# Kernel optimization log

Measured on AMD Instinct MI355X. Metric: run time of the kernel, lower is better.

The kernel has to match this reference:

```python
import jax, jax.numpy as jnp
import numpy as np

C = 128

def setup_inputs() -> dict:
    key = jax.random.key(0)
    ks = jax.random.split(key, 7)
    s = 1.0 / np.sqrt(C)
    return {
        "x": jax.random.normal(ks[0], (8, C, 64, 64), dtype=jnp.float32),
        "Wq": jax.random.uniform(ks[1], (C, C), jnp.float32, -s, s),
        "bq": jax.random.uniform(ks[2], (C,), jnp.float32, -s, s),
        "Wk": jax.random.uniform(ks[3], (C, C), jnp.float32, -s, s),
        "bk": jax.random.uniform(ks[4], (C,), jnp.float32, -s, s),
        "Wv": jax.random.uniform(ks[5], (C, C), jnp.float32, -s, s),
        "bv": jax.random.uniform(ks[6], (C,), jnp.float32, -s, s),
    }

def reference(x, Wq, bq, Wk, bk, Wv, bv):
    bs, c, h, w = x.shape
    xf = x.reshape(bs, c, h * w)                      # [B, C, N]
    # 1x1 convs == per-pixel linear maps over channels
    q = jnp.einsum("dc,bcn->bdn", Wq, xf) + bq[None, :, None]
    k = jnp.einsum("dc,bcn->bdn", Wk, xf) + bk[None, :, None]
    v = jnp.einsum("dc,bcn->bdn", Wv, xf) + bv[None, :, None]
    # energy[b,i,j] = <q[:,i], k[:,j]>  (no 1/sqrt(d) scaling, per original)
    energy = jnp.einsum("bci,bcj->bij", q, k)         # [B, N, N]
    attn = jax.nn.softmax(energy, axis=-1)
    # out[b,c,i] = sum_j v[b,c,j] * attn[b,i,j]
    out = jnp.einsum("bcj,bij->bci", v, attn)
    return out.reshape(bs, c, h, w)
```

## Files before the change

kernel.cpp:

```cpp
#include <hip/hip_runtime.h>
#include <stdint.h>
#include <math.h>

typedef float  f32x2  __attribute__((ext_vector_type(2)));
typedef float  f32x4  __attribute__((ext_vector_type(4)));
typedef float  f32x16 __attribute__((ext_vector_type(16)));
typedef short  bf16x8 __attribute__((ext_vector_type(8)));
typedef unsigned int u32;
typedef unsigned int u32x4 __attribute__((ext_vector_type(4)));
typedef unsigned short ushort_t;

#define MFMA32(a, b, c) __builtin_amdgcn_mfma_f32_32x32x16_bf16((a), (b), (c), 0, 0, 0)

constexpr int B_ = 8, C_ = 128, N_ = 4096;
constexpr float LOG2E = 1.44269504088896340736f;

__device__ __forceinline__ u32 pack2bf(float a, float b) {
  u32 ua = __builtin_bit_cast(u32, a);
  u32 ub = __builtin_bit_cast(u32, b);
  ua += 0x7fffu + ((ua >> 16) & 1u);
  ub += 0x7fffu + ((ub >> 16) & 1u);
  return (ua >> 16) | (ub & 0xffff0000u);
}
__device__ __forceinline__ u32 pkfast(float a, float b) {
  u32 ua = __builtin_bit_cast(u32, a) + 0x8000u;
  u32 ub = __builtin_bit_cast(u32, b) + 0x8000u;
  return __builtin_amdgcn_perm(ub, ua, 0x07060302u);
}
__device__ __forceinline__ bf16x8 pack8(const float* v, float s) {
  u32x4 d = { pack2bf(v[0]*s, v[1]*s), pack2bf(v[2]*s, v[3]*s),
              pack2bf(v[4]*s, v[5]*s), pack2bf(v[6]*s, v[7]*s) };
  return __builtin_bit_cast(bf16x8, d);
}

__device__ __forceinline__ void gload_lds16(const ushort_t* g, ushort_t* l) {
  __builtin_amdgcn_global_load_lds(
      (const __attribute__((address_space(1))) void*)g,
      (__attribute__((address_space(3))) void*)l, 16, 0, 0);
}

__device__ __forceinline__ bf16x8 mk_pa(const f32x16& sv, int rb, float& lacc) {
  float e0 = __builtin_amdgcn_exp2f(sv[rb+0]);
  float e1 = __builtin_amdgcn_exp2f(sv[rb+1]);
  float e2 = __builtin_amdgcn_exp2f(sv[rb+2]);
  float e3 = __builtin_amdgcn_exp2f(sv[rb+3]);
  float e4 = __builtin_amdgcn_exp2f(sv[rb+4]);
  float e5 = __builtin_amdgcn_exp2f(sv[rb+5]);
  float e6 = __builtin_amdgcn_exp2f(sv[rb+6]);
  float e7 = __builtin_amdgcn_exp2f(sv[rb+7]);
  lacc += ((e0+e1)+(e2+e3)) + ((e4+e5)+(e6+e7));
  u32 a  = pkfast(e0, e1), b2 = pkfast(e2, e3);
  u32 c2 = pkfast(e4, e5), d2 = pkfast(e6, e7);
  asm("v_permlane32_swap_b32 %0, %1" : "+v"(a), "+v"(c2));
  asm("v_permlane32_swap_b32 %0, %1" : "+v"(b2), "+v"(d2));
  u32x4 fr = { a, b2, c2, d2 };
  return __builtin_bit_cast(bf16x8, fr);
}

__global__ __launch_bounds__(256)
void wprep_kernel(const float* __restrict__ Wq, const float* __restrict__ Wk,
                  const float* __restrict__ Wv, ushort_t* __restrict__ Wf)
{
  const int tid  = blockIdx.x * 256 + threadIdx.x;
  const int widx = tid >> 11;
  const int r    = tid & 2047;
  const int dt   = r >> 9;
  const int kc   = (r >> 6) & 7;
  const int ln   = r & 63;
  const float* W = (widx == 0) ? Wq : (widx == 1) ? Wk : Wv;
  const float s  = (widx == 0) ? LOG2E : 1.0f;
  const int d    = dt * 32 + (ln & 31);
  const int c0   = kc * 16 + (ln >> 5) * 8;
  const float* p = W + d * C_ + c0;
  f32x4 lo = *(const f32x4*)p, hi = *(const f32x4*)(p + 4);
  float v[8] = { lo.x, lo.y, lo.z, lo.w, hi.x, hi.y, hi.z, hi.w };
  *(bf16x8*)(Wf + (size_t)tid * 8) = pack8(v, s);
}

__global__ __launch_bounds__(256, 3)
void proj_kernel(const float* __restrict__ x,
                 const float* __restrict__ bq, const float* __restrict__ bk,
                 const float* __restrict__ bv, const ushort_t* __restrict__ Wf,
                 ushort_t* __restrict__ Qf, ushort_t* __restrict__ Kf,
                 ushort_t* __restrict__ Vf)
{
  const int b   = blockIdx.x & 7;
  const int nt  = blockIdx.x >> 3;
  const int n0  = nt << 5;
  const int t   = threadIdx.x;
  const int dt  = t >> 6;
  const int lane = t & 63;
  const int l31 = t & 31;
  const int lq1 = (t >> 5) & 1;

  __shared__ float xs[32 * 130];
  {
    const float* xb = x + (size_t)b * C_ * N_ + n0;
    const int m  = t & 7;
    const int cb = t >> 3;
#pragma unroll
    for (int it = 0; it < 4; ++it) {
      const int c = it * 32 + cb;
      f32x4 v = *(const f32x4*)(xb + (size_t)c * N_ + m * 4);
#pragma unroll
      for (int e = 0; e < 4; ++e)
        xs[(m * 4 + e) * 130 + c] = v[e];
    }
  }
  __syncthreads();

  bf16x8 xf[8];
#pragma unroll
  for (int kc = 0; kc < 8; ++kc) {
    const float* row = &xs[l31 * 130 + kc * 16 + lq1 * 8];
    float v[8];
#pragma unroll
    for (int u = 0; u < 4; ++u) {
      f32x2 p = *(const f32x2*)(row + 2 * u);
      v[2*u] = p.x; v[2*u+1] = p.y;
    }
    xf[kc] = pack8(v, 1.0f);
  }

  const ushort_t* WQf = Wf;
  const ushort_t* WKf = Wf + 16384;
  const ushort_t* WVf = Wf + 32768;
  const f32x16 Z = {0,0,0,0,0,0,0,0,0,0,0,0,0,0,0,0};

  f32x16 sq = Z, sk = Z, sv = Z;
#pragma unroll
  for (int kc = 0; kc < 8; ++kc) {
    const size_t wo = (size_t)(dt * 8 + kc) * 512 + lane * 8;
    bf16x8 wq = *(const bf16x8*)(WQf + wo);
    bf16x8 wk = *(const bf16x8*)(WKf + wo);
    bf16x8 wvv = *(const bf16x8*)(WVf + wo);
    sq = MFMA32(wq, xf[kc], sq);
    sk = MFMA32(wk, xf[kc], sk);
    sv = MFMA32(xf[kc], wvv, sv);
  }

#pragma unroll
  for (int q = 0; q < 4; ++q) {
    const int dbase = dt * 32 + q * 8 + lq1 * 4;
    f32x4 b4q = *(const f32x4*)(bq + dbase);
    f32x4 b4k = *(const f32x4*)(bk + dbase);
    uint2 qs, ks;
    qs.x = pack2bf(sq[4*q+0] + b4q.x * LOG2E, sq[4*q+1] + b4q.y * LOG2E);
    qs.y = pack2bf(sq[4*q+2] + b4q.z * LOG2E, sq[4*q+3] + b4q.w * LOG2E);
    ks.x = pack2bf(sk[4*q+0] + b4k.x, sk[4*q+1] + b4k.y);
    ks.y = pack2bf(sk[4*q+2] + b4k.z, sk[4*q+3] + b4k.w);
    const int kcf = dt * 2 + (q >> 1), h = q & 1;
    const size_t off = ((size_t)((b * 128 + nt) * 8 + kcf) * 64 + h * 32 + l31) * 8 + lq1 * 4;
    *(uint2*)(Qf + off) = qs;
    *(uint2*)(Kf + off) = ks;
  }

  {
    const float bvl = bv[dt * 32 + l31];
    const int j64 = nt >> 1, qp = nt & 1;
#pragma unroll
    for (int q = 0; q < 4; ++q) {
      uint2 vs;
      vs.x = pack2bf(sv[4*q+0] + bvl, sv[4*q+1] + bvl);
      vs.y = pack2bf(sv[4*q+2] + bvl, sv[4*q+3] + bvl);
      const int cc = qp * 2 + (q >> 1);
      const size_t off = ((size_t)((b * 64 + j64) * 4 + dt) * 4 + cc) * 512 +
                         (size_t)((q & 1) * 32 + l31) * 8 + lq1 * 4;
      *(uint2*)(Vf + off) = vs;
    }
  }
}

__global__ __launch_bounds__(256, 3)
void flash_kernel(const ushort_t* __restrict__ Qf, const ushort_t* __restrict__ Kf,
                  const ushort_t* __restrict__ Vf, float* __restrict__ out,
                  float* __restrict__ opart, float* __restrict__ lpart, int js)
{
  const int b     = blockIdx.x & 7;
  const int itile = (blockIdx.x >> 3) & 31;
  const int jsl   = blockIdx.x >> 8;
  const int t     = threadIdx.x;
  const int wv    = t >> 6;
  const int lane  = t & 63;
  const int l31   = t & 31;
  const int lq1   = (t >> 5) & 1;
  const int i0    = itile * 128 + wv * 32;

  __shared__ __align__(16) short smem[24576];

  const int jt0 = (jsl * 128) / js;
  const int jt1 = ((jsl + 1) * 128) / js;
  const int NT  = jt1 - jt0;
  const ushort_t* Kt0   = Kf + (size_t)b * 524288;
  const ushort_t* Vbase = Vf + (size_t)b * 524288;

  auto stage = [&](int jt, int p) {
    ushort_t* kb = (ushort_t*)smem + p * 4096;
    ushort_t* vb = (ushort_t*)smem + 12288 + p * 4096;
    const ushort_t* ksrc = Kt0 + (size_t)jt * 4096;
    const int qp = jt & 1;
    const ushort_t* vsrc = Vbase + (size_t)(jt >> 1) * 8192;
#pragma unroll
    for (int c = 0; c < 2; ++c) {
      const int g = wv * 2 + c;
      gload_lds16(ksrc + g * 512 + lane * 8, kb + g * 512);
    }
#pragma unroll
    for (int c = 0; c < 2; ++c) {
      const int h2 = wv * 2 + c;
      const int ct = h2 >> 1, h = h2 & 1;
      gload_lds16(vsrc + (size_t)(ct * 4 + qp * 2 + h) * 512 + lane * 8,
                  vb + h2 * 512);
    }
  };

  bf16x8 qf[8];
  const size_t qb = (size_t)((b * 128 + itile * 4 + wv) * 8) * 512;
#pragma unroll
  for (int kc = 0; kc < 8; ++kc)
    qf[kc] = *(const bf16x8*)(Qf + qb + (size_t)kc * 512 + lane * 8);

  const f32x16 Z = {0,0,0,0,0,0,0,0,0,0,0,0,0,0,0,0};
  f32x16 o[4] = {Z, Z, Z, Z};
  float lsum = 0.f;

  auto qk = [&](const short* kbuf) -> f32x16 {
    f32x16 s = Z;
#pragma unroll
    for (int kc = 0; kc < 8; ++kc) {
      bf16x8 kfr = *(const bf16x8*)&kbuf[kc * 512 + lane * 8];
      s = MFMA32(kfr, qf[kc], s);
    }
    return s;
  };
  auto pv = [&](const short* vbuf, bf16x8 a0, bf16x8 a1) {
#pragma unroll
    for (int ct = 0; ct < 4; ++ct) {
      bf16x8 vf0 = *(const bf16x8*)&vbuf[(ct * 2 + 0) * 512 + lane * 8];
      o[ct] = MFMA32(vf0, a0, o[ct]);
      bf16x8 vf1 = *(const bf16x8*)&vbuf[(ct * 2 + 1) * 512 + lane * 8];
      o[ct] = MFMA32(vf1, a1, o[ct]);
    }
  };

  stage(jt0, 0);
  stage(jt0 + 1, 1);
  asm volatile("s_waitcnt vmcnt(4)" ::: "memory");
  __builtin_amdgcn_sched_barrier(0);
  __builtin_amdgcn_s_barrier();
  __builtin_amdgcn_sched_barrier(0);

  int pcur = 0, pstage = 2;
  for (int n = 0; n < NT; ++n) {
    if (n + 2 < NT) stage(jt0 + n + 2, pstage);
    pstage = (pstage == 2) ? 0 : pstage + 1;
    const short* kb = smem + pcur * 4096;
    const short* vb = smem + 12288 + pcur * 4096;
    pcur = (pcur == 2) ? 0 : pcur + 1;

    __builtin_amdgcn_s_setprio(1);
    f32x16 s = qk(kb);
    __builtin_amdgcn_s_setprio(0);
    bf16x8 pa0 = mk_pa(s, 0, lsum);
    bf16x8 pa1 = mk_pa(s, 8, lsum);
    __builtin_amdgcn_s_setprio(1);
    pv(vb, pa0, pa1);
    __builtin_amdgcn_s_setprio(0);

    if (n + 1 < NT) {
      if (n + 2 < NT) asm volatile("s_waitcnt vmcnt(4)" ::: "memory");
      else            asm volatile("s_waitcnt vmcnt(0)" ::: "memory");
      __builtin_amdgcn_sched_barrier(0);
      __builtin_amdgcn_s_barrier();
      __builtin_amdgcn_sched_barrier(0);
    }
  }

  lsum += __shfl_xor(lsum, 32);
  const int ib = i0 + l31;

  if (js == 1) {
    const float inv = 1.0f / lsum;
#pragma unroll
    for (int ct = 0; ct < 4; ++ct)
#pragma unroll
      for (int rg = 0; rg < 16; ++rg) {
        const int c = ct * 32 + (rg >> 2) * 8 + lq1 * 4 + (rg & 3);
        out[(size_t)(b * C_ + c) * N_ + ib] = o[ct][rg] * inv;
      }
  } else {
    float* op = jsl ? (opart + (size_t)(jsl - 1) * B_ * C_ * N_) : out;
#pragma unroll
    for (int ct = 0; ct < 4; ++ct)
#pragma unroll
      for (int rg = 0; rg < 16; ++rg) {
        const int c = ct * 32 + (rg >> 2) * 8 + lq1 * 4 + (rg & 3);
        op[(size_t)(b * C_ + c) * N_ + ib] = o[ct][rg];
      }
    if (lane < 32)
      lpart[(size_t)jsl * B_ * N_ + (size_t)b * N_ + ib] = lsum;
  }
}

__global__ __launch_bounds__(256)
void combine_kernel(const float* __restrict__ opart, const float* __restrict__ lpart,
                    float* __restrict__ out, int js)
{
  const int t  = blockIdx.x * 256 + threadIdx.x;
  const int n4 = (t & 1023) * 4;
  const int bc = t >> 10;
  const int b  = bc >> 7;
  const size_t off  = (size_t)bc * N_ + n4;
  const size_t loff = (size_t)b * N_ + n4;
  f32x4 os = *(const f32x4*)(out + off);
  f32x4 ls = *(const f32x4*)(lpart + loff);
  for (int s = 1; s < js; ++s) {
    os += *(const f32x4*)(opart + (size_t)(s - 1) * B_ * C_ * N_ + off);
    ls += *(const f32x4*)(lpart + (size_t)s * B_ * N_ + loff);
  }
  f32x4 r = { os.x / ls.x, os.y / ls.y, os.z / ls.z, os.w / ls.w };
  *(f32x4*)(out + off) = r;
}

extern "C" void kernel_launch(void* const* d_in, const int* in_sizes, int n_in,
                              void* d_out, int out_size, void* d_ws, size_t ws_size,
                              hipStream_t stream) {
  const float* x  = (const float*)d_in[0];
  const float* Wq = (const float*)d_in[1];
  const float* bq = (const float*)d_in[2];
  const float* Wk = (const float*)d_in[3];
  const float* bk = (const float*)d_in[4];
  const float* Wv = (const float*)d_in[5];
  const float* bv = (const float*)d_in[6];
  float* out = (float*)d_out;

  const size_t nc = (size_t)B_ * N_ * C_;
  ushort_t* qf = (ushort_t*)d_ws;
  ushort_t* kf = qf + nc;
  ushort_t* vf = kf + nc;
  ushort_t* wf = vf + nc;
  const size_t base = (3 * nc + 49152) * sizeof(ushort_t);

  auto need = [&](int jss) {
    return base + (size_t)jss * (size_t)B_ * N_ * 4 +
           (size_t)(jss - 1) * (size_t)B_ * C_ * N_ * 4;
  };
  const int js = (ws_size >= need(3)) ? 3 : (ws_size >= need(2)) ? 2 : 1;

  float* lpart = (float*)((char*)d_ws + base);
  float* opart = lpart + (size_t)js * B_ * N_;

  hipLaunchKernelGGL(wprep_kernel, dim3(24), dim3(256), 0, stream, Wq, Wk, Wv, wf);
  hipLaunchKernelGGL(proj_kernel, dim3(1024), dim3(256), 0, stream,
                     x, bq, bk, bv, wf, qf, kf, vf);
  hipLaunchKernelGGL(flash_kernel, dim3(256 * js), dim3(256), 0, stream,
                     qf, kf, vf, out, opart, lpart, js);
  if (js > 1)
    hipLaunchKernelGGL(combine_kernel, dim3(4096), dim3(256), 0, stream,
                       opart, lpart, out, js);
}
```

Measured before the change: 169.5 us.

## Process two 32-row query tiles per wave to reuse K/V LDS fragments

Each wave now handles 64 query rows, split into two 32-row halves with separate accumulators and softmax sums. Each K and V fragment read from LDS feeds two MFMAs, which halves LDS traffic per MFMA and doubles the query rows per block. In exchange the grid is halved, the occupancy hint drops from 3 to 2 blocks, register pressure rises, and the key split count goes up to 4 when workspace allows, so the combine pass reads more partials.

Result: faster. 166.1 us (-2.0%).

```diff
diff --git a/kernel.cpp b/kernel.cpp
--- a/kernel.cpp
+++ b/kernel.cpp
@@ -171,20 +171,20 @@
   }
 }
 
-__global__ __launch_bounds__(256, 3)
+__global__ __launch_bounds__(256, 2)
 void flash_kernel(const ushort_t* __restrict__ Qf, const ushort_t* __restrict__ Kf,
                   const ushort_t* __restrict__ Vf, float* __restrict__ out,
                   float* __restrict__ opart, float* __restrict__ lpart, int js)
 {
   const int b     = blockIdx.x & 7;
-  const int itile = (blockIdx.x >> 3) & 31;
-  const int jsl   = blockIdx.x >> 8;
+  const int itile = (blockIdx.x >> 3) & 15;
+  const int jsl   = blockIdx.x >> 7;
   const int t     = threadIdx.x;
   const int wv    = t >> 6;
   const int lane  = t & 63;
   const int l31   = t & 31;
   const int lq1   = (t >> 5) & 1;
-  const int i0    = itile * 128 + wv * 32;
+  const int i0    = itile * 256 + wv * 64;
 
   __shared__ __align__(16) short smem[24576];
 
@@ -214,34 +214,18 @@
     }
   };
 
-  bf16x8 qf[8];
-  const size_t qb = (size_t)((b * 128 + itile * 4 + wv) * 8) * 512;
-#pragma unroll
-  for (int kc = 0; kc < 8; ++kc)
-    qf[kc] = *(const bf16x8*)(Qf + qb + (size_t)kc * 512 + lane * 8);
+  bf16x8 qlo[8], qhi[8];
+  const size_t glo = (size_t)((b * 128 + itile * 8 + wv * 2) * 8) * 512;
+#pragma unroll
+  for (int kc = 0; kc < 8; ++kc) {
+    qlo[kc] = *(const bf16x8*)(Qf + glo + (size_t)kc * 512 + lane * 8);
+    qhi[kc] = *(const bf16x8*)(Qf + glo + 4096 + (size_t)kc * 512 + lane * 8);
+  }
 
   const f32x16 Z = {0,0,0,0,0,0,0,0,0,0,0,0,0,0,0,0};
-  f32x16 o[4] = {Z, Z, Z, Z};
-  float lsum = 0.f;
-
-  auto qk = [&](const short* kbuf) -> f32x16 {
-    f32x16 s = Z;
-#pragma unroll
-    for (int kc = 0; kc < 8; ++kc) {
-      bf16x8 kfr = *(const bf16x8*)&kbuf[kc * 512 + lane * 8];
-      s = MFMA32(kfr, qf[kc], s);
-    }
-    return s;
-  };
-  auto pv = [&](const short* vbuf, bf16x8 a0, bf16x8 a1) {
-#pragma unroll
-    for (int ct = 0; ct < 4; ++ct) {
-      bf16x8 vf0 = *(const bf16x8*)&vbuf[(ct * 2 + 0) * 512 + lane * 8];
-      o[ct] = MFMA32(vf0, a0, o[ct]);
-      bf16x8 vf1 = *(const bf16x8*)&vbuf[(ct * 2 + 1) * 512 + lane * 8];
-      o[ct] = MFMA32(vf1, a1, o[ct]);
-    }
-  };
+  f32x16 olo[4] = {Z, Z, Z, Z};
+  f32x16 ohi[4] = {Z, Z, Z, Z};
+  float lsum_lo = 0.f, lsum_hi = 0.f;
 
   stage(jt0, 0);
   stage(jt0 + 1, 1);
@@ -259,12 +243,28 @@
     pcur = (pcur == 2) ? 0 : pcur + 1;
 
     __builtin_amdgcn_s_setprio(1);
-    f32x16 s = qk(kb);
+    f32x16 slo = Z, shi = Z;
+#pragma unroll
+    for (int kc = 0; kc < 8; ++kc) {
+      bf16x8 kfr = *(const bf16x8*)&kb[kc * 512 + lane * 8];
+      slo = MFMA32(kfr, qlo[kc], slo);
+      shi = MFMA32(kfr, qhi[kc], shi);
+    }
     __builtin_amdgcn_s_setprio(0);
-    bf16x8 pa0 = mk_pa(s, 0, lsum);
-    bf16x8 pa1 = mk_pa(s, 8, lsum);
+    bf16x8 pl0 = mk_pa(slo, 0, lsum_lo);
+    bf16x8 pl1 = mk_pa(slo, 8, lsum_lo);
+    bf16x8 ph0 = mk_pa(shi, 0, lsum_hi);
+    bf16x8 ph1 = mk_pa(shi, 8, lsum_hi);
     __builtin_amdgcn_s_setprio(1);
-    pv(vb, pa0, pa1);
+#pragma unroll
+    for (int ct = 0; ct < 4; ++ct) {
+      bf16x8 vf0 = *(const bf16x8*)&vb[(ct * 2 + 0) * 512 + lane * 8];
+      olo[ct] = MFMA32(vf0, pl0, olo[ct]);
+      ohi[ct] = MFMA32(vf0, ph0, ohi[ct]);
+      bf16x8 vf1 = *(const bf16x8*)&vb[(ct * 2 + 1) * 512 + lane * 8];
+      olo[ct] = MFMA32(vf1, pl1, olo[ct]);
+      ohi[ct] = MFMA32(vf1, ph1, ohi[ct]);
+    }
     __builtin_amdgcn_s_setprio(0);
 
     if (n + 1 < NT) {
@@ -276,17 +276,19 @@
     }
   }
 
-  lsum += __shfl_xor(lsum, 32);
+  lsum_lo += __shfl_xor(lsum_lo, 32);
+  lsum_hi += __shfl_xor(lsum_hi, 32);
   const int ib = i0 + l31;
 
   if (js == 1) {
-    const float inv = 1.0f / lsum;
+    const float invl = 1.0f / lsum_lo, invh = 1.0f / lsum_hi;
 #pragma unroll
     for (int ct = 0; ct < 4; ++ct)
 #pragma unroll
       for (int rg = 0; rg < 16; ++rg) {
         const int c = ct * 32 + (rg >> 2) * 8 + lq1 * 4 + (rg & 3);
-        out[(size_t)(b * C_ + c) * N_ + ib] = o[ct][rg] * inv;
+        out[(size_t)(b * C_ + c) * N_ + ib]      = olo[ct][rg] * invl;
+        out[(size_t)(b * C_ + c) * N_ + ib + 32] = ohi[ct][rg] * invh;
       }
   } else {
     float* op = jsl ? (opart + (size_t)(jsl - 1) * B_ * C_ * N_) : out;
@@ -295,10 +297,13 @@
 #pragma unroll
       for (int rg = 0; rg < 16; ++rg) {
         const int c = ct * 32 + (rg >> 2) * 8 + lq1 * 4 + (rg & 3);
-        op[(size_t)(b * C_ + c) * N_ + ib] = o[ct][rg];
+        op[(size_t)(b * C_ + c) * N_ + ib]      = olo[ct][rg];
+        op[(size_t)(b * C_ + c) * N_ + ib + 32] = ohi[ct][rg];
       }
-    if (lane < 32)
-      lpart[(size_t)jsl * B_ * N_ + (size_t)b * N_ + ib] = lsum;
+    if (lane < 32) {
+      lpart[(size_t)jsl * B_ * N_ + (size_t)b * N_ + ib]      = lsum_lo;
+      lpart[(size_t)jsl * B_ * N_ + (size_t)b * N_ + ib + 32] = lsum_hi;
+    }
   }
 }
 
@@ -345,7 +350,8 @@
     return base + (size_t)jss * (size_t)B_ * N_ * 4 +
            (size_t)(jss - 1) * (size_t)B_ * C_ * N_ * 4;
   };
-  const int js = (ws_size >= need(3)) ? 3 : (ws_size >= need(2)) ? 2 : 1;
+  const int js = (ws_size >= need(4)) ? 4 : (ws_size >= need(3)) ? 3 :
+                 (ws_size >= need(2)) ? 2 : 1;
 
   float* lpart = (float*)((char*)d_ws + base);
   float* opart = lpart + (size_t)js * B_ * N_;
@@ -353,7 +359,7 @@
   hipLaunchKernelGGL(wprep_kernel, dim3(24), dim3(256), 0, stream, Wq, Wk, Wv, wf);
   hipLaunchKernelGGL(proj_kernel, dim3(1024), dim3(256), 0, stream,
                      x, bq, bk, bv, wf, qf, kf, vf);
-  hipLaunchKernelGGL(flash_kernel, dim3(256 * js), dim3(256), 0, stream,
+  hipLaunchKernelGGL(flash_kernel, dim3(128 * js), dim3(256), 0, stream,
                      qf, kf, vf, out, opart, lpart, js);
   if (js > 1)
     hipLaunchKernelGGL(combine_kernel, dim3(4096), dim3(256), 0, stream,
```

## Use 512-thread blocks with staggered wave groups sharing a 4-deep K/V ring

Applied to the files above, without the earlier changes.

The flash kernel moves to 512-thread blocks of 8 waves, each covering 256 query rows. Only the first group of four waves issues the K/V global-to-LDS loads. The second group computes on the same tiles one step behind, so both groups share each staged tile. To keep the reads and writes of the two groups apart, the LDS ring grows to 4 interleaved K/V buffers (64KB), and the KV split drops from 3 to at most 2. This aims to halve K/V traffic per query row and overlap the groups' work, but it lowers resident waves per CU and leaves fewer blocks to spread across CUs.

After: 172.7 us. Within noise of the previous version (+1.9%).

```diff
diff --git a/kernel.cpp b/kernel.cpp
--- a/kernel.cpp
+++ b/kernel.cpp
@@ -171,32 +171,34 @@
   }
 }
 
-__global__ __launch_bounds__(256, 3)
+__global__ __launch_bounds__(512, 2)
 void flash_kernel(const ushort_t* __restrict__ Qf, const ushort_t* __restrict__ Kf,
                   const ushort_t* __restrict__ Vf, float* __restrict__ out,
                   float* __restrict__ opart, float* __restrict__ lpart, int js)
 {
   const int b     = blockIdx.x & 7;
-  const int itile = (blockIdx.x >> 3) & 31;
-  const int jsl   = blockIdx.x >> 8;
+  const int itile = (blockIdx.x >> 3) & 15;
+  const int jsl   = blockIdx.x >> 7;
   const int t     = threadIdx.x;
   const int wv    = t >> 6;
+  const int grp   = wv >> 2;
   const int lane  = t & 63;
   const int l31   = t & 31;
   const int lq1   = (t >> 5) & 1;
-  const int i0    = itile * 128 + wv * 32;
-
-  __shared__ __align__(16) short smem[24576];
-
-  const int jt0 = (jsl * 128) / js;
-  const int jt1 = ((jsl + 1) * 128) / js;
-  const int NT  = jt1 - jt0;
+  const int i0    = itile * 256 + wv * 32;
+
+  __shared__ __align__(16) short smem[32768];
+
+  const int jt0 = jsl * (128 / 2) * (js == 2) + (js == 1 ? 0 : 0);
+  const int NT  = (js == 2) ? 64 : 128;
+  const int base_jt = (js == 2) ? jsl * 64 : 0;
   const ushort_t* Kt0   = Kf + (size_t)b * 524288;
   const ushort_t* Vbase = Vf + (size_t)b * 524288;
+  (void)jt0;
 
   auto stage = [&](int jt, int p) {
-    ushort_t* kb = (ushort_t*)smem + p * 4096;
-    ushort_t* vb = (ushort_t*)smem + 12288 + p * 4096;
+    ushort_t* kb = (ushort_t*)smem + p * 8192;
+    ushort_t* vb = kb + 4096;
     const ushort_t* ksrc = Kt0 + (size_t)jt * 4096;
     const int qp = jt & 1;
     const ushort_t* vsrc = Vbase + (size_t)(jt >> 1) * 8192;
@@ -215,7 +217,7 @@
   };
 
   bf16x8 qf[8];
-  const size_t qb = (size_t)((b * 128 + itile * 4 + wv) * 8) * 512;
+  const size_t qb = (size_t)((b * 128 + itile * 8 + wv) * 8) * 512;
 #pragma unroll
   for (int kc = 0; kc < 8; ++kc)
     qf[kc] = *(const bf16x8*)(Qf + qb + (size_t)kc * 512 + lane * 8);
@@ -224,56 +226,54 @@
   f32x16 o[4] = {Z, Z, Z, Z};
   float lsum = 0.f;
 
-  auto qk = [&](const short* kbuf) -> f32x16 {
+  auto compute = [&](int p) {
+    const short* kb = smem + p * 8192;
+    const short* vb = kb + 4096;
+    __builtin_amdgcn_s_setprio(1);
     f32x16 s = Z;
 #pragma unroll
     for (int kc = 0; kc < 8; ++kc) {
-      bf16x8 kfr = *(const bf16x8*)&kbuf[kc * 512 + lane * 8];
+      bf16x8 kfr = *(const bf16x8*)&kb[kc * 512 + lane * 8];
       s = MFMA32(kfr, qf[kc], s);
     }
-    return s;
-  };
-  auto pv = [&](const short* vbuf, bf16x8 a0, bf16x8 a1) {
-#pragma unroll
-    for (int ct = 0; ct < 4; ++ct) {
-      bf16x8 vf0 = *(const bf16x8*)&vbuf[(ct * 2 + 0) * 512 + lane * 8];
-      o[ct] = MFMA32(vf0, a0, o[ct]);
-      bf16x8 vf1 = *(const bf16x8*)&vbuf[(ct * 2 + 1) * 512 + lane * 8];
-      o[ct] = MFMA32(vf1, a1, o[ct]);
-    }
-  };
-
-  stage(jt0, 0);
-  stage(jt0 + 1, 1);
-  asm volatile("s_waitcnt vmcnt(4)" ::: "memory");
-  __builtin_amdgcn_sched_barrier(0);
-  __builtin_amdgcn_s_barrier();
-  __builtin_amdgcn_sched_barrier(0);
-
-  int pcur = 0, pstage = 2;
-  for (int n = 0; n < NT; ++n) {
-    if (n + 2 < NT) stage(jt0 + n + 2, pstage);
-    pstage = (pstage == 2) ? 0 : pstage + 1;
-    const short* kb = smem + pcur * 4096;
-    const short* vb = smem + 12288 + pcur * 4096;
-    pcur = (pcur == 2) ? 0 : pcur + 1;
-
-    __builtin_amdgcn_s_setprio(1);
-    f32x16 s = qk(kb);
     __builtin_amdgcn_s_setprio(0);
     bf16x8 pa0 = mk_pa(s, 0, lsum);
     bf16x8 pa1 = mk_pa(s, 8, lsum);
     __builtin_amdgcn_s_setprio(1);
-    pv(vb, pa0, pa1);
+#pragma unroll
+    for (int ct = 0; ct < 4; ++ct) {
+      bf16x8 vf0 = *(const bf16x8*)&vb[(ct * 2 + 0) * 512 + lane * 8];
+      o[ct] = MFMA32(vf0, pa0, o[ct]);
+      bf16x8 vf1 = *(const bf16x8*)&vb[(ct * 2 + 1) * 512 + lane * 8];
+      o[ct] = MFMA32(vf1, pa1, o[ct]);
+    }
     __builtin_amdgcn_s_setprio(0);
-
-    if (n + 1 < NT) {
-      if (n + 2 < NT) asm volatile("s_waitcnt vmcnt(4)" ::: "memory");
-      else            asm volatile("s_waitcnt vmcnt(0)" ::: "memory");
-      __builtin_amdgcn_sched_barrier(0);
-      __builtin_amdgcn_s_barrier();
-      __builtin_amdgcn_sched_barrier(0);
-    }
+  };
+
+  asm volatile("s_waitcnt vmcnt(0)" ::: "memory");
+  if (grp == 0) {
+    stage(base_jt + 0, 0);
+    stage(base_jt + 1, 1);
+    asm volatile("s_waitcnt vmcnt(4)" ::: "memory");
+  }
+  __builtin_amdgcn_sched_barrier(0);
+  __builtin_amdgcn_s_barrier();
+  __builtin_amdgcn_sched_barrier(0);
+
+  for (int s = 0; s <= NT; ++s) {
+    if (grp == 0) {
+      if (s < NT) {
+        if (s + 2 < NT) stage(base_jt + s + 2, (s + 2) & 3);
+        compute(s & 3);
+        if (s + 2 < NT) asm volatile("s_waitcnt vmcnt(4)" ::: "memory");
+        else            asm volatile("s_waitcnt vmcnt(0)" ::: "memory");
+      }
+    } else {
+      if (s >= 1) compute((s - 1) & 3);
+    }
+    __builtin_amdgcn_sched_barrier(0);
+    __builtin_amdgcn_s_barrier();
+    __builtin_amdgcn_sched_barrier(0);
   }
 
   lsum += __shfl_xor(lsum, 32);
@@ -345,7 +345,7 @@
     return base + (size_t)jss * (size_t)B_ * N_ * 4 +
            (size_t)(jss - 1) * (size_t)B_ * C_ * N_ * 4;
   };
-  const int js = (ws_size >= need(3)) ? 3 : (ws_size >= need(2)) ? 2 : 1;
+  const int js = (ws_size >= need(2)) ? 2 : 1;
 
   float* lpart = (float*)((char*)d_ws + base);
   float* opart = lpart + (size_t)js * B_ * N_;
@@ -353,7 +353,7 @@
   hipLaunchKernelGGL(wprep_kernel, dim3(24), dim3(256), 0, stream, Wq, Wk, Wv, wf);
   hipLaunchKernelGGL(proj_kernel, dim3(1024), dim3(256), 0, stream,
                      x, bq, bk, bv, wf, qf, kf, vf);
-  hipLaunchKernelGGL(flash_kernel, dim3(256 * js), dim3(256), 0, stream,
+  hipLaunchKernelGGL(flash_kernel, dim3(128 * js), dim3(512), 0, stream,
                      qf, kf, vf, out, opart, lpart, js);
   if (js > 1)
     hipLaunchKernelGGL(combine_kernel, dim3(4096), dim3(256), 0, stream,
```

## Process two KV tiles per barrier with 4-slot LDS ring and split-2

Applied to the files above, without the earlier changes.

Restructures the flash attention main loop to stage and compute two K/V tiles per iteration using a 4-slot shared memory ring, halving the number of workgroup barriers and waitcnts. LDS grows from 48KB to 64KB and launch bounds drop from 3 to 2 blocks per CU. The split count along keys is capped at 2 instead of 3, reducing combine work but lowering grid parallelism. The loop assumes an even tile count per split (NT>>1), which holds for 128/2=64 and 128/1=128 but would silently drop a tile for odd counts.

New measurement: 166.3 us. Within noise of the previous version (-1.9%).

```diff
diff --git a/kernel.cpp b/kernel.cpp
--- a/kernel.cpp
+++ b/kernel.cpp
@@ -171,7 +171,7 @@
   }
 }
 
-__global__ __launch_bounds__(256, 3)
+__global__ __launch_bounds__(256, 2)
 void flash_kernel(const ushort_t* __restrict__ Qf, const ushort_t* __restrict__ Kf,
                   const ushort_t* __restrict__ Vf, float* __restrict__ out,
                   float* __restrict__ opart, float* __restrict__ lpart, int js)
@@ -186,7 +186,7 @@
   const int lq1   = (t >> 5) & 1;
   const int i0    = itile * 128 + wv * 32;
 
-  __shared__ __align__(16) short smem[24576];
+  __shared__ __align__(16) short smem[32768];
 
   const int jt0 = (jsl * 128) / js;
   const int jt1 = ((jsl + 1) * 128) / js;
@@ -196,7 +196,7 @@
 
   auto stage = [&](int jt, int p) {
     ushort_t* kb = (ushort_t*)smem + p * 4096;
-    ushort_t* vb = (ushort_t*)smem + 12288 + p * 4096;
+    ushort_t* vb = (ushort_t*)smem + 16384 + p * 4096;
     const ushort_t* ksrc = Kt0 + (size_t)jt * 4096;
     const int qp = jt & 1;
     const ushort_t* vsrc = Vbase + (size_t)(jt >> 1) * 8192;
@@ -224,52 +224,49 @@
   f32x16 o[4] = {Z, Z, Z, Z};
   float lsum = 0.f;
 
-  auto qk = [&](const short* kbuf) -> f32x16 {
+  auto compute = [&](int p) {
+    const short* kb = smem + p * 4096;
+    const short* vb = smem + 16384 + p * 4096;
+    __builtin_amdgcn_s_setprio(1);
     f32x16 s = Z;
 #pragma unroll
     for (int kc = 0; kc < 8; ++kc) {
-      bf16x8 kfr = *(const bf16x8*)&kbuf[kc * 512 + lane * 8];
+      bf16x8 kfr = *(const bf16x8*)&kb[kc * 512 + lane * 8];
       s = MFMA32(kfr, qf[kc], s);
     }
-    return s;
-  };
-  auto pv = [&](const short* vbuf, bf16x8 a0, bf16x8 a1) {
-#pragma unroll
-    for (int ct = 0; ct < 4; ++ct) {
-      bf16x8 vf0 = *(const bf16x8*)&vbuf[(ct * 2 + 0) * 512 + lane * 8];
-      o[ct] = MFMA32(vf0, a0, o[ct]);
-      bf16x8 vf1 = *(const bf16x8*)&vbuf[(ct * 2 + 1) * 512 + lane * 8];
-      o[ct] = MFMA32(vf1, a1, o[ct]);
-    }
-  };
-
-  stage(jt0, 0);
-  stage(jt0 + 1, 1);
-  asm volatile("s_waitcnt vmcnt(4)" ::: "memory");
-  __builtin_amdgcn_sched_barrier(0);
-  __builtin_amdgcn_s_barrier();
-  __builtin_amdgcn_sched_barrier(0);
-
-  int pcur = 0, pstage = 2;
-  for (int n = 0; n < NT; ++n) {
-    if (n + 2 < NT) stage(jt0 + n + 2, pstage);
-    pstage = (pstage == 2) ? 0 : pstage + 1;
-    const short* kb = smem + pcur * 4096;
-    const short* vb = smem + 12288 + pcur * 4096;
-    pcur = (pcur == 2) ? 0 : pcur + 1;
-
-    __builtin_amdgcn_s_setprio(1);
-    f32x16 s = qk(kb);
     __builtin_amdgcn_s_setprio(0);
     bf16x8 pa0 = mk_pa(s, 0, lsum);
     bf16x8 pa1 = mk_pa(s, 8, lsum);
     __builtin_amdgcn_s_setprio(1);
-    pv(vb, pa0, pa1);
+#pragma unroll
+    for (int ct = 0; ct < 4; ++ct) {
+      bf16x8 vf0 = *(const bf16x8*)&vb[(ct * 2 + 0) * 512 + lane * 8];
+      o[ct] = MFMA32(vf0, pa0, o[ct]);
+      bf16x8 vf1 = *(const bf16x8*)&vb[(ct * 2 + 1) * 512 + lane * 8];
+      o[ct] = MFMA32(vf1, pa1, o[ct]);
+    }
     __builtin_amdgcn_s_setprio(0);
-
-    if (n + 1 < NT) {
-      if (n + 2 < NT) asm volatile("s_waitcnt vmcnt(4)" ::: "memory");
-      else            asm volatile("s_waitcnt vmcnt(0)" ::: "memory");
+  };
+
+  stage(jt0 + 0, 0);
+  stage(jt0 + 1, 1);
+  asm volatile("s_waitcnt vmcnt(0)" ::: "memory");
+  __builtin_amdgcn_sched_barrier(0);
+  __builtin_amdgcn_s_barrier();
+  __builtin_amdgcn_sched_barrier(0);
+
+  const int NS = NT >> 1;
+  for (int s = 0; s < NS; ++s) {
+    const int t2 = jt0 + 2 * s;
+    const bool more = (s + 1 < NS);
+    if (more) {
+      stage(t2 + 2, (2 * s + 2) & 3);
+      stage(t2 + 3, (2 * s + 3) & 3);
+    }
+    compute((2 * s) & 3);
+    compute((2 * s + 1) & 3);
+    if (more) {
+      asm volatile("s_waitcnt vmcnt(0)" ::: "memory");
       __builtin_amdgcn_sched_barrier(0);
       __builtin_amdgcn_s_barrier();
       __builtin_amdgcn_sched_barrier(0);
@@ -345,7 +342,7 @@
     return base + (size_t)jss * (size_t)B_ * N_ * 4 +
            (size_t)(jss - 1) * (size_t)B_ * C_ * N_ * 4;
   };
-  const int js = (ws_size >= need(3)) ? 3 : (ws_size >= need(2)) ? 2 : 1;
+  const int js = (ws_size >= need(2)) ? 2 : 1;
 
   float* lpart = (float*)((char*)d_ws + base);
   float* opart = lpart + (size_t)js * B_ * N_;
```
